# Performance work log

Hardware: AMD Instinct MI355X
Metric: run time of the kernel (lower is better)

Reference implementation:

```python
import jax, jax.numpy as jnp
import numpy as np

B, T = 64, 2048
D_RNN, D_EMB, D_ATT = 1024, 512, 128
N_FILT, KSIZE = 32, 31
PAD = (KSIZE - 1) // 2


def setup_inputs() -> dict:
    key = jax.random.key(0)
    ks = jax.random.split(key, 9)
    return {
        "attention_hidden_state": jax.random.normal(ks[0], (B, D_RNN), jnp.float32),
        "memory": jax.random.normal(ks[1], (B, T, D_EMB), jnp.float32),
        "processed_memory": jax.random.normal(ks[2], (B, T, D_ATT), jnp.float32),
        "attention_weights_cat": jax.random.uniform(ks[3], (B, 2, T), jnp.float32),
        "mask": jax.random.randint(ks[4], (B, T), 0, 2) > 0,
        # learned params (all bias-free, as in the torch module)
        "Wq": jax.random.normal(ks[5], (D_ATT, D_RNN), jnp.float32) * 0.02,   # query_layer.weight
        "Wv": jax.random.normal(ks[6], (1, D_ATT), jnp.float32) * 0.02,        # v.weight
        "conv_w": jax.random.normal(ks[7], (N_FILT, 2, KSIZE), jnp.float32) * 0.1,  # location_conv.weight (OIH)
        "Wd": jax.random.normal(ks[8], (D_ATT, N_FILT), jnp.float32) * 0.02,   # location_dense.weight
    }


def reference(attention_hidden_state, memory, processed_memory,
              attention_weights_cat, mask, Wq, Wv, conv_w, Wd):
    # processed query: [B, 1, D_ATT]
    pq = (attention_hidden_state @ Wq.T)[:, None, :]
    # location features: Conv1d(2 -> N_FILT, same padding) over time
    loc = jax.lax.conv_general_dilated(
        attention_weights_cat, conv_w,
        window_strides=(1,), padding=[(PAD, PAD)],
        dimension_numbers=("NCH", "OIH", "NCH"))           # [B, N_FILT, T]
    paw = jnp.einsum("bft,af->bta", loc, Wd)               # [B, T, D_ATT]
    # additive energies -> scalar per position via v-projection
    energies = jnp.einsum("bta,a->bt", jnp.tanh(pq + paw + processed_memory), Wv[0])
    alignment = jnp.where(mask, -jnp.inf, energies)         # masked fill
    attention_weights = jax.nn.softmax(alignment, axis=1)   # [B, T]
    attention_context = jnp.einsum("bt,btd->bd", attention_weights, memory)  # [B, D_EMB]
    return attention_context, jax.lax.stop_gradient(attention_weights)
```

## Files before the change

### kernel.cpp

```cpp
#include <hip/hip_runtime.h>
#include <math.h>

#define B_    64
#define T_    2048
#define DRNN  1024
#define DEMB  512
#define DATT  128
#define NF    32
#define KS    31
#define PADL  15
#define MP    64
#define TT    32
#define CT    64
#define NC    (T_/CT)

__device__ __forceinline__ float fast_tanh(float x){
    float e2 = __expf(2.0f * x);
    return 1.0f - 2.0f / (e2 + 1.0f);
}

__global__ __launch_bounds__(128) void prep_kernel(
    const float* __restrict__ hidden, const float* __restrict__ Wq,
    const float* __restrict__ Wd, const float* __restrict__ convw,
    float* __restrict__ pq, float* __restrict__ M)
{
    const int blk = blockIdx.x;
    const int a = threadIdx.x;
    if (blk < B_) {
        __shared__ float sh[DRNN];
        const int b = blk;
        #pragma unroll
        for (int i = 0; i < DRNN/128; ++i) sh[a + 128*i] = hidden[b*DRNN + a + 128*i];
        __syncthreads();
        const float4* wq4 = (const float4*)(Wq + a*DRNN);
        float acc = 0.f;
        #pragma unroll 4
        for (int k = 0; k < DRNN/4; ++k){
            float4 w = wq4[k];
            acc = fmaf(w.x, sh[4*k+0], acc);
            acc = fmaf(w.y, sh[4*k+1], acc);
            acc = fmaf(w.z, sh[4*k+2], acc);
            acc = fmaf(w.w, sh[4*k+3], acc);
        }
        pq[b*DATT + a] = acc;
    } else {
        float wd[NF];
        #pragma unroll
        for (int f = 0; f < NF; ++f) wd[f] = Wd[a*NF + f];
        for (int ck = 0; ck < 2*KS; ++ck){
            float acc = 0.f;
            #pragma unroll
            for (int f = 0; f < NF; ++f) acc = fmaf(wd[f], convw[f*2*KS + ck], acc);
            M[a*MP + ck] = acc;
        }
    }
}

__global__ __launch_bounds__(256) void fused_kernel(
    const float* __restrict__ pm, const float* __restrict__ awcat,
    const float* __restrict__ pq, const float* __restrict__ M,
    const float* __restrict__ Wv, const int* __restrict__ mask,
    const float* __restrict__ memory,
    float* __restrict__ pbuf, float* __restrict__ pmax,
    float* __restrict__ psum, float* __restrict__ pctx)
{
    const int b   = blockIdx.y;
    const int cx  = blockIdx.x;
    const int t0  = cx * CT;
    const int tid = threadIdx.x;
    const int s   = tid >> 7;
    const int a   = tid & 127;
    const int ts  = t0 + TT * s;

    __shared__ float saw0[96], saw1[96];
    __shared__ float sred[2][2][TT];
    __shared__ float sp[CT];
    __shared__ float4 sacc[128];

    for (int i = tid; i < 94; i += 256){
        int tt = t0 - PADL + i;
        bool ok = (tt >= 0) && (tt < T_);
        saw0[i] = ok ? awcat[(b*2+0)*T_ + tt] : 0.f;
        saw1[i] = ok ? awcat[(b*2+1)*T_ + tt] : 0.f;
    }
    __syncthreads();

    float Ma0[KS], Ma1[KS];
    const float* Mrow = M + a*MP;
    #pragma unroll
    for (int k = 0; k < KS; ++k){ Ma0[k] = Mrow[k]; Ma1[k] = Mrow[KS + k]; }
    const float pqa = pq[b*DATT + a];
    const float wv  = Wv[a];

    float acc[TT];
    #pragma unroll
    for (int t = 0; t < TT; ++t) acc[t] = pqa;

    #pragma unroll
    for (int j = 0; j < TT + KS - 1; ++j){
        const float av0 = saw0[j + TT*s];
        const float av1 = saw1[j + TT*s];
        const int tlo = (j - KS + 1) > 0 ? (j - KS + 1) : 0;
        const int thi = (j < TT - 1) ? j : (TT - 1);
        #pragma unroll
        for (int t = tlo; t <= thi; ++t){
            acc[t] = fmaf(Ma0[j - t], av0, acc[t]);
            acc[t] = fmaf(Ma1[j - t], av1, acc[t]);
        }
    }

    const float* pmb = pm + ((size_t)(b*T_ + ts)) * DATT + a;
    #pragma unroll
    for (int t = 0; t < TT; ++t){
        float x = acc[t] + pmb[(size_t)t * DATT];
        acc[t] = wv * fast_tanh(x);
    }

    const int lane = tid & 63;
    const int half = a >> 6;
    #pragma unroll
    for (int t = 0; t < TT; ++t){
        float r = acc[t];
        r += __shfl_xor(r, 1, 64);  r += __shfl_xor(r, 2, 64);
        r += __shfl_xor(r, 4, 64);  r += __shfl_xor(r, 8, 64);
        r += __shfl_xor(r, 16, 64); r += __shfl_xor(r, 32, 64);
        if (lane == 0) sred[s][half][t] = r;
    }
    __syncthreads();

    if (tid < 64){
        const int t = t0 + tid;
        float e = sred[tid>>5][0][tid&31] + sred[tid>>5][1][tid&31];
        const int mk = mask[b*T_ + t];
        float mval = mk ? -1e30f : e;
        #pragma unroll
        for (int off = 1; off < 64; off <<= 1) mval = fmaxf(mval, __shfl_xor(mval, off, 64));
        const float pval = mk ? 0.f : __expf(e - mval);
        float sv = pval;
        #pragma unroll
        for (int off = 1; off < 64; off <<= 1) sv += __shfl_xor(sv, off, 64);
        sp[tid] = pval;
        pbuf[b*T_ + t] = pval;
        if (tid == 0){
            pmax[b*NC + cx] = mval;
            psum[b*NC + cx] = sv;
        }
    }
    __syncthreads();

    const int col = tid & 127;
    const int row = tid >> 7;
    float4 a4 = make_float4(0.f, 0.f, 0.f, 0.f);
    const float4* mem4 = (const float4*)memory + ((size_t)(b*T_ + t0))*(DEMB/4) + col;
    for (int tt = row; tt < CT; tt += 2){
        const float w = sp[tt];
        if (w != 0.f){
            const float4 m = mem4[(size_t)tt * (DEMB/4)];
            a4.x = fmaf(w, m.x, a4.x);
            a4.y = fmaf(w, m.y, a4.y);
            a4.z = fmaf(w, m.z, a4.z);
            a4.w = fmaf(w, m.w, a4.w);
        }
    }
    if (row == 1) sacc[col] = a4;
    __syncthreads();
    if (row == 0){
        const float4 o = sacc[col];
        float4* dst = (float4*)(pctx + ((size_t)(b*NC + cx))*DEMB) + col;
        *dst = make_float4(a4.x + o.x, a4.y + o.y, a4.z + o.z, a4.w + o.w);
    }
}

__global__ __launch_bounds__(256) void finalize_kernel(
    const float* __restrict__ pbuf, const float* __restrict__ pmax,
    const float* __restrict__ psum, const float* __restrict__ pctx,
    float* __restrict__ ctx, float* __restrict__ wout)
{
    const int b = blockIdx.x;
    const int tid = threadIdx.x;
    __shared__ float sscale[NC];

    if (tid < 64){
        float mv = (tid < NC) ? pmax[b*NC + tid] : -1e30f;
        float sv = (tid < NC) ? psum[b*NC + tid] : 0.f;
        float g = mv;
        #pragma unroll
        for (int off = 1; off < 64; off <<= 1) g = fmaxf(g, __shfl_xor(g, off, 64));
        float z = sv * __expf(mv - g);
        #pragma unroll
        for (int off = 1; off < 64; off <<= 1) z += __shfl_xor(z, off, 64);
        if (tid < NC) sscale[tid] = __expf(mv - g) / z;
    }
    __syncthreads();

    float2 a2 = make_float2(0.f, 0.f);
    const float2* pc2 = (const float2*)(pctx + (size_t)b*NC*DEMB) + tid;
    #pragma unroll
    for (int c = 0; c < NC; ++c){
        const float sc = sscale[c];
        if (sc != 0.f){
            const float2 v = pc2[(size_t)c * (DEMB/2)];
            a2.x = fmaf(sc, v.x, a2.x);
            a2.y = fmaf(sc, v.y, a2.y);
        }
    }
    ((float2*)(ctx + b*DEMB))[tid] = a2;

    #pragma unroll
    for (int i = 0; i < T_/256; ++i){
        const int t = tid + 256*i;
        wout[b*T_ + t] = pbuf[b*T_ + t] * sscale[t >> 6];
    }
}

extern "C" void kernel_launch(void* const* d_in, const int* in_sizes, int n_in,
                              void* d_out, int out_size, void* d_ws, size_t ws_size,
                              hipStream_t stream)
{
    const float* hidden = (const float*)d_in[0];
    const float* memory = (const float*)d_in[1];
    const float* pm     = (const float*)d_in[2];
    const float* awcat  = (const float*)d_in[3];
    const int*   mask   = (const int*)d_in[4];
    const float* Wq     = (const float*)d_in[5];
    const float* Wv     = (const float*)d_in[6];
    const float* convw  = (const float*)d_in[7];
    const float* Wd     = (const float*)d_in[8];

    float* out  = (float*)d_out;
    float* ctx  = out;
    float* wout = out + B_*DEMB;

    float* pq    = (float*)d_ws;
    float* M     = pq   + B_*DATT;
    float* pbuf  = M    + DATT*MP;
    float* pmax  = pbuf + B_*T_;
    float* psum  = pmax + B_*NC;
    float* pctx  = psum + B_*NC;

    prep_kernel<<<dim3(B_ + 1), 128, 0, stream>>>(hidden, Wq, Wd, convw, pq, M);
    fused_kernel<<<dim3(NC, B_), 256, 0, stream>>>(pm, awcat, pq, M, Wv, mask,
                                                   memory, pbuf, pmax, psum, pctx);
    finalize_kernel<<<dim3(B_), 256, 0, stream>>>(pbuf, pmax, psum, pctx, ctx, wout);
}
```

Baseline: 484.0 us.

## Split fused attention kernel, skip masked processed_memory loads, split-K query projection

```diff
diff --git a/kernel.cpp b/kernel.cpp
--- a/kernel.cpp
+++ b/kernel.cpp
@@ -19,35 +19,43 @@
     return 1.0f - 2.0f / (e2 + 1.0f);
 }
 
-__global__ __launch_bounds__(128) void prep_kernel(
+__global__ __launch_bounds__(256) void prep_kernel(
     const float* __restrict__ hidden, const float* __restrict__ Wq,
     const float* __restrict__ Wd, const float* __restrict__ convw,
     float* __restrict__ pq, float* __restrict__ M)
 {
     const int blk = blockIdx.x;
-    const int a = threadIdx.x;
+    const int tid = threadIdx.x;
     if (blk < B_) {
         __shared__ float sh[DRNN];
+        __shared__ float part[DATT];
         const int b = blk;
         #pragma unroll
-        for (int i = 0; i < DRNN/128; ++i) sh[a + 128*i] = hidden[b*DRNN + a + 128*i];
+        for (int i = 0; i < DRNN/256; ++i) sh[tid + 256*i] = hidden[b*DRNN + tid + 256*i];
         __syncthreads();
-        const float4* wq4 = (const float4*)(Wq + a*DRNN);
+        const int a = tid & 127;
+        const int h = tid >> 7;
+        const float4* wq4 = (const float4*)(Wq + a*DRNN + h*(DRNN/2));
+        const float*  shh = sh + h*(DRNN/2);
         float acc = 0.f;
-        #pragma unroll 4
-        for (int k = 0; k < DRNN/4; ++k){
+        #pragma unroll 8
+        for (int k = 0; k < DRNN/8; ++k){
             float4 w = wq4[k];
-            acc = fmaf(w.x, sh[4*k+0], acc);
-            acc = fmaf(w.y, sh[4*k+1], acc);
-            acc = fmaf(w.z, sh[4*k+2], acc);
-            acc = fmaf(w.w, sh[4*k+3], acc);
-        }
-        pq[b*DATT + a] = acc;
+            acc = fmaf(w.x, shh[4*k+0], acc);
+            acc = fmaf(w.y, shh[4*k+1], acc);
+            acc = fmaf(w.z, shh[4*k+2], acc);
+            acc = fmaf(w.w, shh[4*k+3], acc);
+        }
+        if (h) part[a] = acc;
+        __syncthreads();
+        if (!h) pq[b*DATT + a] = acc + part[a];
     } else {
+        const int a = tid & 127;
+        const int h = tid >> 7;
         float wd[NF];
         #pragma unroll
         for (int f = 0; f < NF; ++f) wd[f] = Wd[a*NF + f];
-        for (int ck = 0; ck < 2*KS; ++ck){
+        for (int ck = h*KS; ck < h*KS + KS; ++ck){
             float acc = 0.f;
             #pragma unroll
             for (int f = 0; f < NF; ++f) acc = fmaf(wd[f], convw[f*2*KS + ck], acc);
@@ -56,13 +64,12 @@
     }
 }
 
-__global__ __launch_bounds__(256) void fused_kernel(
+__global__ __launch_bounds__(256) void energy_kernel(
     const float* __restrict__ pm, const float* __restrict__ awcat,
     const float* __restrict__ pq, const float* __restrict__ M,
     const float* __restrict__ Wv, const int* __restrict__ mask,
-    const float* __restrict__ memory,
     float* __restrict__ pbuf, float* __restrict__ pmax,
-    float* __restrict__ psum, float* __restrict__ pctx)
+    float* __restrict__ psum)
 {
     const int b   = blockIdx.y;
     const int cx  = blockIdx.x;
@@ -74,8 +81,6 @@
 
     __shared__ float saw0[96], saw1[96];
     __shared__ float sred[2][2][TT];
-    __shared__ float sp[CT];
-    __shared__ float4 sacc[128];
 
     for (int i = tid; i < 94; i += 256){
         int tt = t0 - PADL + i;
@@ -85,6 +90,15 @@
     }
     __syncthreads();
 
+    const float* pmb  = pm + ((size_t)(b*T_ + ts)) * DATT + a;
+    const int*   mrow = mask + b*T_ + ts;
+    float pmv[TT];
+    #pragma unroll
+    for (int t = 0; t < TT; ++t){
+        int mk = __builtin_amdgcn_readfirstlane(mrow[t]);
+        pmv[t] = mk ? 0.f : pmb[(size_t)t * DATT];
+    }
+
     float Ma0[KS], Ma1[KS];
     const float* Mrow = M + a*MP;
     #pragma unroll
@@ -109,11 +123,9 @@
         }
     }
 
-    const float* pmb = pm + ((size_t)(b*T_ + ts)) * DATT + a;
     #pragma unroll
     for (int t = 0; t < TT; ++t){
-        float x = acc[t] + pmb[(size_t)t * DATT];
-        acc[t] = wv * fast_tanh(x);
+        acc[t] = wv * fast_tanh(acc[t] + pmv[t]);
     }
 
     const int lane = tid & 63;
@@ -139,12 +151,46 @@
         float sv = pval;
         #pragma unroll
         for (int off = 1; off < 64; off <<= 1) sv += __shfl_xor(sv, off, 64);
-        sp[tid] = pval;
         pbuf[b*T_ + t] = pval;
         if (tid == 0){
             pmax[b*NC + cx] = mval;
             psum[b*NC + cx] = sv;
         }
+    }
+}
+
+__global__ __launch_bounds__(256) void ctx_kernel(
+    const float* __restrict__ pbuf, const float* __restrict__ pmax,
+    const float* __restrict__ psum, const float* __restrict__ memory,
+    float* __restrict__ pctx, float* __restrict__ wout)
+{
+    const int b   = blockIdx.y;
+    const int cx  = blockIdx.x;
+    const int t0  = cx * CT;
+    const int tid = threadIdx.x;
+
+    __shared__ float sw[CT];
+    __shared__ float4 sacc[128];
+    __shared__ float s_scale;
+
+    if (tid < 64){
+        float mv = (tid < NC) ? pmax[b*NC + tid] : -1e30f;
+        float sv = (tid < NC) ? psum[b*NC + tid] : 0.f;
+        float g = mv;
+        #pragma unroll
+        for (int off = 1; off < 64; off <<= 1) g = fmaxf(g, __shfl_xor(g, off, 64));
+        float z = sv * __expf(mv - g);
+        #pragma unroll
+        for (int off = 1; off < 64; off <<= 1) z += __shfl_xor(z, off, 64);
+        if (tid == cx) s_scale = __expf(mv - g) / z;
+    }
+    __syncthreads();
+    const float sc = s_scale;
+
+    if (tid < CT){
+        const float w = pbuf[b*T_ + t0 + tid] * sc;
+        sw[tid] = w;
+        wout[b*T_ + t0 + tid] = w;
     }
     __syncthreads();
 
@@ -153,7 +199,7 @@
     float4 a4 = make_float4(0.f, 0.f, 0.f, 0.f);
     const float4* mem4 = (const float4*)memory + ((size_t)(b*T_ + t0))*(DEMB/4) + col;
     for (int tt = row; tt < CT; tt += 2){
-        const float w = sp[tt];
+        const float w = sw[tt];
         if (w != 0.f){
             const float4 m = mem4[(size_t)tt * (DEMB/4)];
             a4.x = fmaf(w, m.x, a4.x);
@@ -172,45 +218,19 @@
 }
 
 __global__ __launch_bounds__(256) void finalize_kernel(
-    const float* __restrict__ pbuf, const float* __restrict__ pmax,
-    const float* __restrict__ psum, const float* __restrict__ pctx,
-    float* __restrict__ ctx, float* __restrict__ wout)
+    const float* __restrict__ pctx, float* __restrict__ ctx)
 {
     const int b = blockIdx.x;
     const int tid = threadIdx.x;
-    __shared__ float sscale[NC];
-
-    if (tid < 64){
-        float mv = (tid < NC) ? pmax[b*NC + tid] : -1e30f;
-        float sv = (tid < NC) ? psum[b*NC + tid] : 0.f;
-        float g = mv;
-        #pragma unroll
-        for (int off = 1; off < 64; off <<= 1) g = fmaxf(g, __shfl_xor(g, off, 64));
-        float z = sv * __expf(mv - g);
-        #pragma unroll
-        for (int off = 1; off < 64; off <<= 1) z += __shfl_xor(z, off, 64);
-        if (tid < NC) sscale[tid] = __expf(mv - g) / z;
-    }
-    __syncthreads();
-
     float2 a2 = make_float2(0.f, 0.f);
     const float2* pc2 = (const float2*)(pctx + (size_t)b*NC*DEMB) + tid;
     #pragma unroll
     for (int c = 0; c < NC; ++c){
-        const float sc = sscale[c];
-        if (sc != 0.f){
-            const float2 v = pc2[(size_t)c * (DEMB/2)];
-            a2.x = fmaf(sc, v.x, a2.x);
-            a2.y = fmaf(sc, v.y, a2.y);
-        }
+        const float2 v = pc2[(size_t)c * (DEMB/2)];
+        a2.x += v.x;
+        a2.y += v.y;
     }
     ((float2*)(ctx + b*DEMB))[tid] = a2;
-
-    #pragma unroll
-    for (int i = 0; i < T_/256; ++i){
-        const int t = tid + 256*i;
-        wout[b*T_ + t] = pbuf[b*T_ + t] * sscale[t >> 6];
-    }
 }
 
 extern "C" void kernel_launch(void* const* d_in, const int* in_sizes, int n_in,
@@ -238,8 +258,10 @@
     float* psum  = pmax + B_*NC;
     float* pctx  = psum + B_*NC;
 
-    prep_kernel<<<dim3(B_ + 1), 128, 0, stream>>>(hidden, Wq, Wd, convw, pq, M);
-    fused_kernel<<<dim3(NC, B_), 256, 0, stream>>>(pm, awcat, pq, M, Wv, mask,
-                                                   memory, pbuf, pmax, psum, pctx);
-    finalize_kernel<<<dim3(B_), 256, 0, stream>>>(pbuf, pmax, psum, pctx, ctx, wout);
-}
+    prep_kernel<<<dim3(B_ + 1), 256, 0, stream>>>(hidden, Wq, Wd, convw, pq, M);
+    energy_kernel<<<dim3(NC, B_), 256, 0, stream>>>(pm, awcat, pq, M, Wv, mask,
+                                                    pbuf, pmax, psum);
+    ctx_kernel<<<dim3(NC, B_), 256, 0, stream>>>(pbuf, pmax, psum, memory,
+                                                 pctx, wout);
+    finalize_kernel<<<dim3(B_), 256, 0, stream>>>(pctx, ctx);
+}
```

After: 541.5 us. 1.12x slower.
